# Performance work log

Hardware: AMD Instinct MI355X
Metric: run time of the kernel (lower is better)

## Reference

```python
import jax, jax.numpy as jnp
import numpy as np

ALPHA = 0.25
GAMMA = 2.0
EPS = 1e-8


def _lsa(cost):
    """Jonker-Volgenant shortest-augmenting-path linear sum assignment.
    Matches scipy.optimize.linear_sum_assignment for rectangular matrices."""
    cost = np.asarray(cost, dtype=np.float64)
    transposed = cost.shape[0] > cost.shape[1]
    if transposed:
        cost = cost.T
    n, m = cost.shape  # n <= m
    INF = 1e18
    u = np.zeros(n + 1)
    v = np.zeros(m + 1)
    p = np.zeros(m + 1, dtype=np.int64)   # p[j] = row (1-indexed) assigned to col j
    way = np.zeros(m + 1, dtype=np.int64)
    for i in range(1, n + 1):
        p[0] = i
        j0 = 0
        minv = np.full(m + 1, INF)
        used = np.zeros(m + 1, dtype=bool)
        while True:
            used[j0] = True
            i0 = p[j0]
            cur = cost[i0 - 1] - u[i0] - v[1:]
            free = ~used[1:]
            better = free & (cur < minv[1:])
            minv[1:][better] = cur[better]
            way[1:][better] = j0
            masked = np.where(free, minv[1:], INF)
            j1 = int(np.argmin(masked)) + 1
            delta = masked[j1 - 1]
            u[p[used]] += delta
            v[used] -= delta
            minv[1:][free] -= delta
            j0 = j1
            if p[j0] == 0:
                break
        while j0 != 0:  # augment
            j1 = way[j0]
            p[j0] = p[j1]
            j0 = j1
    row_of_col = p[1:] - 1
    cols = np.nonzero(row_of_col >= 0)[0]
    rows = row_of_col[cols]
    if transposed:
        rows, cols = cols, rows
    order = np.argsort(rows)
    return rows[order], cols[order]


def _focal_cost(p):
    """pos_cost - neg_cost for sigmoid probs p, per focal-loss matcher cost."""
    neg = (1.0 - ALPHA) * p ** GAMMA * (-jnp.log(1.0 - p + EPS))
    pos = ALPHA * (1.0 - p) ** GAMMA * (-jnp.log(p + EPS))
    return pos - neg


def _match(rec, loc, targets):
    """rec: [bs, Q, Crec] logits; loc: [bs, Q, Cloc] logits; targets: [bs, nt] int.
    Returns (src_idx, tgt_idx) each [bs, nt] (query index, target index)."""
    nt = targets.shape[1]
    cost_class = jnp.take_along_axis(_focal_cost(jax.nn.sigmoid(rec)),
                                     targets[:, None, :], axis=2)      # [bs, Q, nt]
    cost_pos = _focal_cost(jax.nn.sigmoid(loc))[:, :, :nt]             # tgt_pos = arange(nt)
    C = np.asarray(2.0 * cost_class + cost_pos)                        # [bs, Q, nt]
    src, tgt = [], []
    for b in range(C.shape[0]):  # per-batch Hungarian, as in original
        r, c = _lsa(C[b])
        src.append(r)
        tgt.append(c)
    return jnp.asarray(np.stack(src)), jnp.asarray(np.stack(tgt))


def _ce(logits, labels):
    # F.cross_entropy with mean reduction
    logp = jax.nn.log_softmax(logits, axis=-1)
    return -jnp.mean(jnp.take_along_axis(logp, labels[..., None], axis=-1))


def setup_inputs() -> dict:
    key = jax.random.key(0)
    k1, k2, k3 = jax.random.split(key, 3)
    rec = jax.random.normal(k1, (128, 107, 32, 32), dtype=jnp.float32)
    loc = jax.random.normal(k2, (128, 25, 32, 32), dtype=jnp.float32)
    targets = jax.random.randint(k3, (128, 25), 0, 107, dtype=jnp.int64)
    return {"rec": rec, "loc": loc, "targets": targets}


def reference(rec, loc, targets):
    bs, c_rec, H, W = rec.shape
    c_loc = loc.shape[1]
    nt = targets.shape[1]
    rec = jnp.transpose(rec.reshape(bs, c_rec, H * W), (0, 2, 1))  # [bs, Q, Crec]
    loc = jnp.transpose(loc.reshape(bs, c_loc, H * W), (0, 2, 1))  # [bs, Q, Cloc]
    src_idx, tgt_idx = _match(rec, loc, targets)                   # [bs, nt] each
    rec_m = jnp.take_along_axis(rec, src_idx[:, :, None], axis=1)  # [bs, nt, Crec]
    loc_m = jnp.take_along_axis(loc, src_idx[:, :, None], axis=1)  # [bs, nt, Cloc]
    cls_labels = jnp.take_along_axis(targets, tgt_idx, axis=1)     # [bs, nt]
    pos_labels = tgt_idx                                           # tgt_pos[b, j] == j
    det_rec_losses = _ce(rec_m.reshape(bs * nt, c_rec), cls_labels.reshape(-1))
    pos_losses = _ce(loc_m.reshape(bs * nt, c_loc), pos_labels.reshape(-1))
    return (det_rec_losses, pos_losses)
```

## Files before the change

kernel.cpp:

```cpp
#include <hip/hip_runtime.h>
#include <hip/hip_bf16.h>
#include <math.h>

#define BS   128
#define NT   25
#define CREC 107
#define CLOC 25
#define QN   1024
#define INFD 1e18
#define WSTR 257
__device__ __forceinline__ int widx(int j) {
    int q = j - 1;
    return (q & 3) * WSTR + (q >> 2);
}

__device__ __forceinline__ float focal_cost_f(float x) {
    float p   = 1.0f / (1.0f + __expf(-x));
    float neg = 0.75f * p * p * (-__logf(1.0f - p + 1e-8f));
    float pos = 0.25f * (1.0f - p) * (1.0f - p) * (-__logf(p + 1e-8f));
    return pos - neg;
}

__global__ __launch_bounds__(256)
void rowmin_kernel(const float* __restrict__ rec, const float* __restrict__ loc,
                   const int* __restrict__ targets, float* __restrict__ cost_g,
                   float* __restrict__ rowmin_g, int* __restrict__ rowarg_g) {
    const int pid   = blockIdx.x;
    const int b     = pid / NT, r = pid % NT;
    const int tid   = threadIdx.x;
    const int qbase = tid << 2;
    const int tc    = targets[pid];

    float4 r4 = *(const float4*)(rec + ((size_t)b * CREC + tc) * QN + qbase);
    float4 l4 = *(const float4*)(loc + ((size_t)b * CLOC + r)  * QN + qbase);
    float4 c;
    c.x = 2.0f * focal_cost_f(r4.x) + focal_cost_f(l4.x);
    c.y = 2.0f * focal_cost_f(r4.y) + focal_cost_f(l4.y);
    c.z = 2.0f * focal_cost_f(r4.z) + focal_cost_f(l4.z);
    c.w = 2.0f * focal_cost_f(r4.w) + focal_cost_f(l4.w);
    *(float4*)(cost_g + ((size_t)pid << 10) + qbase) = c;

    float bv = c.x; int bq = qbase;
    if (c.y < bv) { bv = c.y; bq = qbase + 1; }
    if (c.z < bv) { bv = c.z; bq = qbase + 2; }
    if (c.w < bv) { bv = c.w; bq = qbase + 3; }
    #pragma unroll
    for (int off = 32; off; off >>= 1) {
        float ov = __shfl_xor(bv, off);
        int   oq = __shfl_xor(bq, off);
        if (ov < bv || (ov == bv && oq < bq)) { bv = ov; bq = oq; }
    }
    __shared__ float bmv[4];
    __shared__ int   bmq[4];
    if ((tid & 63) == 0) { bmv[tid >> 6] = bv; bmq[tid >> 6] = bq; }
    __syncthreads();
    if (tid == 0) {
        float fv = bmv[0]; int fq = bmq[0];
        #pragma unroll
        for (int w = 1; w < 4; ++w) {
            float ov = bmv[w]; int oq = bmq[w];
            if (ov < fv || (ov == fv && oq < fq)) { fv = ov; fq = oq; }
        }
        rowmin_g[pid] = fv; rowarg_g[pid] = fq;
    }
}

#define SMEM_BYTES 111232

__global__ __launch_bounds__(256)
void search_kernel(const float* __restrict__ cost_g,
                   const float* __restrict__ rowmin_g, const int* __restrict__ rowarg_g,
                   int* __restrict__ pairq_g) {
    const int b     = blockIdx.x;
    const int tid   = threadIdx.x;
    const int wave  = tid >> 6;
    const int lane  = tid & 63;
    const int qbase = tid << 2;

    extern __shared__ char smem_raw[];
    float*  cost_s       = (float*) (smem_raw);
    double* u_s          = (double*)(smem_raw + 102400);
    double* candv_s      = (double*)(smem_raw + 102608);
    int*    way_s        = (int*)   (smem_raw + 102672);
    int*    p_s          = (int*)   (smem_raw + 106784);
    float*  rowmin_s     = (float*) (smem_raw + 110884);
    int*    rowarg_s     = (int*)   (smem_raw + 110984);
    int*    unassigned_s = (int*)   (smem_raw + 111084);
    int*    candj_s      = (int*)   (smem_raw + 111184);
    int*    nun_p        = (int*)   (smem_raw + 111216);

    for (int j = tid; j <= QN; j += 256) p_s[j] = 0;
    if (tid < NT) {
        rowmin_s[tid] = rowmin_g[b * NT + tid];
        rowarg_s[tid] = rowarg_g[b * NT + tid];
    }
    __syncthreads();

    if (tid == 0) {
        int nun = 0;
        for (int r = 0; r < NT; ++r) {
            u_s[r + 1] = (double)rowmin_s[r];
            int j = rowarg_s[r] + 1;
            if (p_s[j] == 0) p_s[j] = r + 1;
            else             unassigned_s[nun++] = r + 1;
        }
        nun_p[0] = nun;
    }
    __syncthreads();
    const int nun = nun_p[0];

    if (nun > 0) {
        const float4* src = (const float4*)(cost_g + ((size_t)b * NT << 10));
        float4*       dst = (float4*)cost_s;
        #pragma unroll 5
        for (int idx = tid; idx < NT * 256; idx += 256) dst[idx] = src[idx];
        __syncthreads();

        double v[4] = {0.0, 0.0, 0.0, 0.0};

        for (int s = 0; s < nun; ++s) {
            const int i = unassigned_s[s];
            double minv[4] = {INFD, INFD, INFD, INFD};
            double snap[4] = {0.0, 0.0, 0.0, 0.0};
            double dsum    = 0.0;
            unsigned usedmask = 0;
            int j0 = 0;
            int parity = 0;

            for (;;) {
                int i0;
                if (j0 == 0) {
                    i0 = i;
                } else {
                    int q0 = j0 - 1;
                    if ((q0 >> 2) == tid) {
                        int m = q0 & 3;
                        usedmask |= 1u << m;
                        minv[m] = INFD;
                        snap[m] = dsum;
                    }
                    i0 = p_s[j0];
                }
                const double ui0 = u_s[i0];
                const float4 c4 = *(const float4*)(cost_s + ((i0 - 1) << 10) + qbase);
                const float cf[4] = { c4.x, c4.y, c4.z, c4.w };

                double bestv = INFD; int bestj = QN + 2;
                #pragma unroll
                for (int m = 0; m < 4; ++m) {
                    if (!(usedmask & (1u << m))) {
                        const int j = qbase + m + 1;
                        double cur = (double)cf[m] - ui0 - v[m];
                        if (cur < minv[m]) { minv[m] = cur; way_s[widx(j)] = j0; }
                        double mv = minv[m];
                        if (mv < bestv || (mv == bestv && j < bestj)) { bestv = mv; bestj = j; }
                    }
                }

                float own32 = (float)bestv;
                float w32 = own32;
                #pragma unroll
                for (int off = 32; off; off >>= 1) w32 = fminf(w32, __shfl_xor(w32, off));
                unsigned long long cand = __ballot(own32 == w32);
                double wv = INFD; int wj = QN + 2;
                while (cand) {
                    int l = __ffsll(cand) - 1; cand &= cand - 1;
                    double vv = __shfl(bestv, l);
                    int    jj = __shfl(bestj, l);
                    if (vv < wv || (vv == wv && jj < wj)) { wv = vv; wj = jj; }
                }
                if (lane == 0) { candv_s[parity * 4 + wave] = wv; candj_s[parity * 4 + wave] = wj; }
                __syncthreads();
                double delta = candv_s[parity * 4]; int j1 = candj_s[parity * 4];
                #pragma unroll
                for (int w = 1; w < 4; ++w) {
                    double dv = candv_s[parity * 4 + w]; int dj = candj_s[parity * 4 + w];
                    if (dv < delta || (dv == delta && dj < j1)) { delta = dv; j1 = dj; }
                }
                parity ^= 1;
                dsum += delta;

                #pragma unroll
                for (int m = 0; m < 4; ++m) {
                    if (usedmask & (1u << m)) v[m]    -= delta;
                    else                      minv[m] -= delta;
                }
                j0 = j1;
                if (p_s[j0] == 0) break;
            }

            if (tid == 0) u_s[i] += dsum;
            unsigned mm = usedmask;
            while (mm) {
                int m = __ffs(mm) - 1; mm &= mm - 1;
                u_s[p_s[qbase + m + 1]] += dsum - snap[m];
            }
            __syncthreads();
            if (tid == 0) {
                int jj = j0;
                while (jj != 0) {
                    int jn = way_s[widx(jj)];
                    p_s[jj] = (jn == 0) ? i : p_s[jn];
                    jj = jn;
                }
            }
            __syncthreads();
        }
    }

    for (int j = tid + 1; j <= QN; j += 256)
        if (p_s[j] > 0) pairq_g[b * NT + (p_s[j] - 1)] = j - 1;
}

__global__ __launch_bounds__(64)
void loss_kernel(const float* __restrict__ rec, const float* __restrict__ loc,
                 const int* __restrict__ targets, const int* __restrict__ pairq_g,
                 float* __restrict__ partial) {
    const int pid  = blockIdx.x;
    const int b    = pid / NT, t = pid % NT;
    const int lane = threadIdx.x;
    const int q    = pairq_g[pid];

    const float* rb = rec + (size_t)b * CREC * QN + q;
    float x0 = (lane < CREC)      ? rb[(size_t)lane * QN]        : -1e30f;
    float x1 = (lane + 64 < CREC) ? rb[(size_t)(lane + 64) * QN] : -1e30f;
    float mx = fmaxf(x0, x1);
    #pragma unroll
    for (int off = 32; off; off >>= 1) mx = fmaxf(mx, __shfl_xor(mx, off));
    float e = 0.0f;
    if (lane < CREC)      e += expf(x0 - mx);
    if (lane + 64 < CREC) e += expf(x1 - mx);
    #pragma unroll
    for (int off = 32; off; off >>= 1) e += __shfl_xor(e, off);
    float lse = mx + logf(e);

    const float* lb = loc + (size_t)b * CLOC * QN + q;
    float y = (lane < CLOC) ? lb[(size_t)lane * QN] : -1e30f;
    float my = y;
    #pragma unroll
    for (int off = 32; off; off >>= 1) my = fmaxf(my, __shfl_xor(my, off));
    float ey = (lane < CLOC) ? expf(y - my) : 0.0f;
    #pragma unroll
    for (int off = 32; off; off >>= 1) ey += __shfl_xor(ey, off);
    float lsey = my + logf(ey);

    if (lane == 0) {
        int lab = targets[pid];
        partial[pid]           = lse  - rb[(size_t)lab * QN];
        partial[BS * NT + pid] = lsey - lb[(size_t)t * QN];
    }
}

__global__ __launch_bounds__(256)
void finalize_kernel(const float* __restrict__ partial, float* __restrict__ out) {
    const int tid = threadIdx.x;
    float s0 = 0.0f, s1 = 0.0f;
    for (int i = tid; i < BS * NT; i += 256) {
        s0 += partial[i];
        s1 += partial[BS * NT + i];
    }
    __shared__ float a0[4], a1[4];
    #pragma unroll
    for (int off = 32; off; off >>= 1) { s0 += __shfl_xor(s0, off); s1 += __shfl_xor(s1, off); }
    if ((tid & 63) == 0) { a0[tid >> 6] = s0; a1[tid >> 6] = s1; }
    __syncthreads();
    if (tid == 0) {
        out[0] = (a0[0] + a0[1] + a0[2] + a0[3]) * (1.0f / (BS * NT));
        out[1] = (a1[0] + a1[1] + a1[2] + a1[3]) * (1.0f / (BS * NT));
    }
}

extern "C" void kernel_launch(void* const* d_in, const int* in_sizes, int n_in,
                              void* d_out, int out_size, void* d_ws, size_t ws_size,
                              hipStream_t stream) {
    (void)in_sizes; (void)n_in; (void)out_size; (void)ws_size;
    const float* rec     = (const float*)d_in[0];
    const float* loc     = (const float*)d_in[1];
    const int*   targets = (const int*)d_in[2];
    float* out = (float*)d_out;

    float* cost_g   = (float*)d_ws;
    float* rowmin_g = cost_g + (size_t)BS * NT * QN;
    int*   rowarg_g = (int*)(rowmin_g + BS * NT);
    int*   pairq_g  = rowarg_g + BS * NT;
    float* partial  = (float*)(pairq_g + BS * NT);

    static bool attr_set = false;
    if (!attr_set) {
        (void)hipFuncSetAttribute((const void*)search_kernel,
                                  hipFuncAttributeMaxDynamicSharedMemorySize,
                                  SMEM_BYTES);
        attr_set = true;
    }

    hipLaunchKernelGGL(rowmin_kernel, dim3(BS * NT), dim3(256), 0, stream,
                       rec, loc, targets, cost_g, rowmin_g, rowarg_g);
    hipLaunchKernelGGL(search_kernel, dim3(BS), dim3(256), SMEM_BYTES, stream,
                       cost_g, rowmin_g, rowarg_g, pairq_g);
    hipLaunchKernelGGL(loss_kernel, dim3(BS * NT), dim3(64), 0, stream,
                       rec, loc, targets, pairq_g, partial);
    hipLaunchKernelGGL(finalize_kernel, dim3(1), dim3(256), 0, stream,
                       partial, out);
}
```

Baseline: 146.2 us.

## Fuse cost computation into matcher and finalize into loss via atomic ticket

The per-row cost and row-minimum computation moves into the per-batch matcher kernel, which writes costs straight into shared memory instead of round-tripping through a global cost buffer. The final reduction now runs in the last-finishing loss block, selected by an atomic counter, which removes a separate launch. Together these cut the launch count from four to two and drop the global cost write and reread. In exchange, cost computation now runs on only 128 blocks instead of 3200, which reduces parallelism for that phase.

```diff
diff --git a/kernel.cpp b/kernel.cpp
--- a/kernel.cpp
+++ b/kernel.cpp
@@ -21,56 +21,12 @@
     return pos - neg;
 }
 
+#define SMEM_BYTES 112128
+
 __global__ __launch_bounds__(256)
-void rowmin_kernel(const float* __restrict__ rec, const float* __restrict__ loc,
-                   const int* __restrict__ targets, float* __restrict__ cost_g,
-                   float* __restrict__ rowmin_g, int* __restrict__ rowarg_g) {
-    const int pid   = blockIdx.x;
-    const int b     = pid / NT, r = pid % NT;
-    const int tid   = threadIdx.x;
-    const int qbase = tid << 2;
-    const int tc    = targets[pid];
-
-    float4 r4 = *(const float4*)(rec + ((size_t)b * CREC + tc) * QN + qbase);
-    float4 l4 = *(const float4*)(loc + ((size_t)b * CLOC + r)  * QN + qbase);
-    float4 c;
-    c.x = 2.0f * focal_cost_f(r4.x) + focal_cost_f(l4.x);
-    c.y = 2.0f * focal_cost_f(r4.y) + focal_cost_f(l4.y);
-    c.z = 2.0f * focal_cost_f(r4.z) + focal_cost_f(l4.z);
-    c.w = 2.0f * focal_cost_f(r4.w) + focal_cost_f(l4.w);
-    *(float4*)(cost_g + ((size_t)pid << 10) + qbase) = c;
-
-    float bv = c.x; int bq = qbase;
-    if (c.y < bv) { bv = c.y; bq = qbase + 1; }
-    if (c.z < bv) { bv = c.z; bq = qbase + 2; }
-    if (c.w < bv) { bv = c.w; bq = qbase + 3; }
-    #pragma unroll
-    for (int off = 32; off; off >>= 1) {
-        float ov = __shfl_xor(bv, off);
-        int   oq = __shfl_xor(bq, off);
-        if (ov < bv || (ov == bv && oq < bq)) { bv = ov; bq = oq; }
-    }
-    __shared__ float bmv[4];
-    __shared__ int   bmq[4];
-    if ((tid & 63) == 0) { bmv[tid >> 6] = bv; bmq[tid >> 6] = bq; }
-    __syncthreads();
-    if (tid == 0) {
-        float fv = bmv[0]; int fq = bmq[0];
-        #pragma unroll
-        for (int w = 1; w < 4; ++w) {
-            float ov = bmv[w]; int oq = bmq[w];
-            if (ov < fv || (ov == fv && oq < fq)) { fv = ov; fq = oq; }
-        }
-        rowmin_g[pid] = fv; rowarg_g[pid] = fq;
-    }
-}
-
-#define SMEM_BYTES 111232
-
-__global__ __launch_bounds__(256)
-void search_kernel(const float* __restrict__ cost_g,
-                   const float* __restrict__ rowmin_g, const int* __restrict__ rowarg_g,
-                   int* __restrict__ pairq_g) {
+void matcher_kernel(const float* __restrict__ rec, const float* __restrict__ loc,
+                    const int* __restrict__ targets, int* __restrict__ pairq_g,
+                    int* __restrict__ counter_g) {
     const int b     = blockIdx.x;
     const int tid   = threadIdx.x;
     const int wave  = tid >> 6;
@@ -85,14 +41,54 @@
     int*    p_s          = (int*)   (smem_raw + 106784);
     float*  rowmin_s     = (float*) (smem_raw + 110884);
     int*    rowarg_s     = (int*)   (smem_raw + 110984);
-    int*    unassigned_s = (int*)   (smem_raw + 111084);
+    int*    tcs_s        = (int*)   (smem_raw + 111084);
     int*    candj_s      = (int*)   (smem_raw + 111184);
     int*    nun_p        = (int*)   (smem_raw + 111216);
+    float*  wpv_s        = (float*) (smem_raw + 111220);
+    int*    wpa_s        = (int*)   (smem_raw + 111620);
+    int*    unassigned_s = (int*)   (smem_raw + 112020);
+
+    if (b == 0 && tid == 0) counter_g[0] = 0;
 
     for (int j = tid; j <= QN; j += 256) p_s[j] = 0;
+    if (tid < NT) tcs_s[tid] = targets[b * NT + tid];
+    __syncthreads();
+
+    const float* recb = rec + (size_t)b * CREC * QN;
+    const float* locb = loc + (size_t)b * CLOC * QN;
+    #pragma unroll 5
+    for (int r = 0; r < NT; ++r) {
+        const int tc = tcs_s[r];
+        float4 r4 = *(const float4*)(recb + ((size_t)tc << 10) + qbase);
+        float4 l4 = *(const float4*)(locb + ((size_t)r  << 10) + qbase);
+        float4 c;
+        c.x = 2.0f * focal_cost_f(r4.x) + focal_cost_f(l4.x);
+        c.y = 2.0f * focal_cost_f(r4.y) + focal_cost_f(l4.y);
+        c.z = 2.0f * focal_cost_f(r4.z) + focal_cost_f(l4.z);
+        c.w = 2.0f * focal_cost_f(r4.w) + focal_cost_f(l4.w);
+        *(float4*)(cost_s + (r << 10) + qbase) = c;
+
+        float bv = c.x; int bq = qbase;
+        if (c.y < bv) { bv = c.y; bq = qbase + 1; }
+        if (c.z < bv) { bv = c.z; bq = qbase + 2; }
+        if (c.w < bv) { bv = c.w; bq = qbase + 3; }
+        #pragma unroll
+        for (int off = 32; off; off >>= 1) {
+            float ov = __shfl_xor(bv, off);
+            int   oq = __shfl_xor(bq, off);
+            if (ov < bv || (ov == bv && oq < bq)) { bv = ov; bq = oq; }
+        }
+        if (lane == 0) { wpv_s[wave * NT + r] = bv; wpa_s[wave * NT + r] = bq; }
+    }
+    __syncthreads();
     if (tid < NT) {
-        rowmin_s[tid] = rowmin_g[b * NT + tid];
-        rowarg_s[tid] = rowarg_g[b * NT + tid];
+        float fv = wpv_s[tid]; int fq = wpa_s[tid];
+        #pragma unroll
+        for (int w = 1; w < 4; ++w) {
+            float ov = wpv_s[w * NT + tid]; int oq = wpa_s[w * NT + tid];
+            if (ov < fv || (ov == fv && oq < fq)) { fv = ov; fq = oq; }
+        }
+        rowmin_s[tid] = fv; rowarg_s[tid] = fq;
     }
     __syncthreads();
 
@@ -110,12 +106,6 @@
     const int nun = nun_p[0];
 
     if (nun > 0) {
-        const float4* src = (const float4*)(cost_g + ((size_t)b * NT << 10));
-        float4*       dst = (float4*)cost_s;
-        #pragma unroll 5
-        for (int idx = tid; idx < NT * 256; idx += 256) dst[idx] = src[idx];
-        __syncthreads();
-
         double v[4] = {0.0, 0.0, 0.0, 0.0};
 
         for (int s = 0; s < nun; ++s) {
@@ -215,7 +205,8 @@
 __global__ __launch_bounds__(64)
 void loss_kernel(const float* __restrict__ rec, const float* __restrict__ loc,
                  const int* __restrict__ targets, const int* __restrict__ pairq_g,
-                 float* __restrict__ partial) {
+                 float* __restrict__ partial, int* __restrict__ counter_g,
+                 float* __restrict__ out) {
     const int pid  = blockIdx.x;
     const int b    = pid / NT, t = pid % NT;
     const int lane = threadIdx.x;
@@ -249,24 +240,32 @@
         partial[pid]           = lse  - rb[(size_t)lab * QN];
         partial[BS * NT + pid] = lsey - lb[(size_t)t * QN];
     }
-}
-
-__global__ __launch_bounds__(256)
-void finalize_kernel(const float* __restrict__ partial, float* __restrict__ out) {
-    const int tid = threadIdx.x;
-    float s0 = 0.0f, s1 = 0.0f;
-    for (int i = tid; i < BS * NT; i += 256) {
-        s0 += partial[i];
-        s1 += partial[BS * NT + i];
-    }
-    __shared__ float a0[4], a1[4];
-    #pragma unroll
-    for (int off = 32; off; off >>= 1) { s0 += __shfl_xor(s0, off); s1 += __shfl_xor(s1, off); }
-    if ((tid & 63) == 0) { a0[tid >> 6] = s0; a1[tid >> 6] = s1; }
-    __syncthreads();
-    if (tid == 0) {
-        out[0] = (a0[0] + a0[1] + a0[2] + a0[3]) * (1.0f / (BS * NT));
-        out[1] = (a1[0] + a1[1] + a1[2] + a1[3]) * (1.0f / (BS * NT));
+
+    __threadfence();
+    int tk = 0;
+    if (lane == 0) tk = atomicAdd(counter_g, 1);
+    tk = __shfl(tk, 0);
+    if (tk == BS * NT - 1) {
+        __threadfence();
+        float fs0[4], fs1[4];
+        #pragma unroll
+        for (int w = 0; w < 4; ++w) {
+            float s0 = 0.0f, s1 = 0.0f;
+            for (int i = w * 64 + lane; i < BS * NT; i += 256) {
+                s0 += partial[i];
+                s1 += partial[BS * NT + i];
+            }
+            #pragma unroll
+            for (int off = 32; off; off >>= 1) {
+                s0 += __shfl_xor(s0, off);
+                s1 += __shfl_xor(s1, off);
+            }
+            fs0[w] = s0; fs1[w] = s1;
+        }
+        if (lane == 0) {
+            out[0] = (((fs0[0] + fs0[1]) + fs0[2]) + fs0[3]) * (1.0f / (BS * NT));
+            out[1] = (((fs1[0] + fs1[1]) + fs1[2]) + fs1[3]) * (1.0f / (BS * NT));
+        }
     }
 }
 
@@ -279,26 +278,20 @@
     const int*   targets = (const int*)d_in[2];
     float* out = (float*)d_out;
 
-    float* cost_g   = (float*)d_ws;
-    float* rowmin_g = cost_g + (size_t)BS * NT * QN;
-    int*   rowarg_g = (int*)(rowmin_g + BS * NT);
-    int*   pairq_g  = rowarg_g + BS * NT;
-    float* partial  = (float*)(pairq_g + BS * NT);
+    int*   pairq_g   = (int*)d_ws;
+    float* partial   = (float*)(pairq_g + BS * NT);
+    int*   counter_g = (int*)(partial + 2 * BS * NT);
 
     static bool attr_set = false;
     if (!attr_set) {
-        (void)hipFuncSetAttribute((const void*)search_kernel,
+        (void)hipFuncSetAttribute((const void*)matcher_kernel,
                                   hipFuncAttributeMaxDynamicSharedMemorySize,
                                   SMEM_BYTES);
         attr_set = true;
     }
 
-    hipLaunchKernelGGL(rowmin_kernel, dim3(BS * NT), dim3(256), 0, stream,
-                       rec, loc, targets, cost_g, rowmin_g, rowarg_g);
-    hipLaunchKernelGGL(search_kernel, dim3(BS), dim3(256), SMEM_BYTES, stream,
-                       cost_g, rowmin_g, rowarg_g, pairq_g);
+    hipLaunchKernelGGL(matcher_kernel, dim3(BS), dim3(256), SMEM_BYTES, stream,
+                       rec, loc, targets, pairq_g, counter_g);
     hipLaunchKernelGGL(loss_kernel, dim3(BS * NT), dim3(64), 0, stream,
-                       rec, loc, targets, pairq_g, partial);
-    hipLaunchKernelGGL(finalize_kernel, dim3(1), dim3(256), 0, stream,
-                       partial, out);
-}
+                       rec, loc, targets, pairq_g, partial, counter_g, out);
+}
```

Result: slower. 292.4 us (+100.0%).
